# Optimization experiments

Hardware: AMD Instinct MI355X
Metric: run time of the kernel (lower is better)

## Reference

```python
import jax, jax.numpy as jnp
import numpy as np

LAYER_NUM = 2
NUM_CLS = 128
HIDDEN = 256
NUM_NODES = 1024


def setup_inputs() -> dict:
    key = jax.random.key(0)
    ks = jax.random.split(key, 12)
    s = 0.05
    return {
        "x": jax.random.normal(ks[0], (NUM_NODES, HIDDEN), jnp.float32),
        "knowledge": jax.random.uniform(ks[1], (NUM_CLS, NUM_CLS), jnp.float32) / NUM_CLS,
        "w3w": jax.random.normal(ks[2], (HIDDEN, 2 * HIDDEN), jnp.float32) * s,
        "b3w": jax.random.normal(ks[3], (HIDDEN,), jnp.float32) * s,
        "u3": jax.random.normal(ks[4], (HIDDEN, HIDDEN), jnp.float32) * s,
        "bu3": jax.random.normal(ks[5], (HIDDEN,), jnp.float32) * s,
        "w4w": jax.random.normal(ks[6], (HIDDEN, 2 * HIDDEN), jnp.float32) * s,
        "b4w": jax.random.normal(ks[7], (HIDDEN,), jnp.float32) * s,
        "w5w": jax.random.normal(ks[8], (HIDDEN, 2 * HIDDEN), jnp.float32) * s,
        "b5w": jax.random.normal(ks[9], (HIDDEN,), jnp.float32) * s,
        "u5": jax.random.normal(ks[10], (HIDDEN, HIDDEN), jnp.float32) * s,
        "bu5": jax.random.normal(ks[11], (HIDDEN,), jnp.float32) * s,
    }


def reference(x, knowledge, w3w, b3w, u3, bu3, w4w, b4w, w5w, b5w, u5, bu5):
    N, H = x.shape
    C = knowledge.shape[0]
    # hidden[n, c, :] = x[n, :]  (repeat per class)
    hidden = jnp.broadcast_to(x[:, None, :], (N, C, H))
    for _ in range(LAYER_NUM):
        hs = hidden.sum(0)                      # [C, H]
        diff = hs[None, :, :] - hidden          # [N, C, H]
        # knowledge.T @ diff_n  and  knowledge @ diff_n, vectorized over nodes
        left = jnp.einsum('kc,nkh->nch', knowledge, diff)
        right = jnp.einsum('ck,nkh->nch', knowledge, diff)
        av = jnp.concatenate([left, right], axis=-1).reshape(N * C, 2 * H)
        h = hidden.reshape(N * C, H)
        uh3 = h @ u3.T + bu3                    # shared: rv uses fc_eq3_u (source quirk)
        zv = jax.nn.sigmoid(av @ w3w.T + b3w + uh3)
        rv = jax.nn.sigmoid(av @ w4w.T + b4w + uh3)
        hv = jnp.tanh(av @ w5w.T + b5w + (rv * h) @ u5.T + bu5)
        h = (1.0 - zv) * h + zv * hv
        hidden = h.reshape(N, C, H)
    return hidden
```

## Files before the change

kernel.cpp:

```cpp
#include <hip/hip_runtime.h>
#include <cstdint>
#include <cstddef>


#define NODES 1024
#define NCLS  128
#define HID   256

using frag  = __attribute__((ext_vector_type(8))) short;
using frag4 = __attribute__((ext_vector_type(4))) short;
using f32x4 = __attribute__((ext_vector_type(4))) float;

__device__ __forceinline__ float bf2f(unsigned short h){
  unsigned int u = ((unsigned int)h) << 16;
  float f; __builtin_memcpy(&f, &u, 4); return f;
}
__device__ __forceinline__ unsigned short f2bf(float f){
  unsigned int u; __builtin_memcpy(&u, &f, 4);
  u = (u + 0x7fffu + ((u >> 16) & 1u)) >> 16;
  return (unsigned short)u;
}
__device__ __forceinline__ float sigm(float x){ return 1.0f/(1.0f + __expf(-x)); }
__device__ __forceinline__ float tanh_fast(float x){ return 1.0f - 2.0f/(__expf(2.0f*x) + 1.0f); }

#define GLOBAL_AS(p) ((const __attribute__((address_space(1))) void*)(p))
#define LDS_AS(p)    ((__attribute__((address_space(3))) void*)(p))

template<int OUT_BF16>
__global__ __launch_bounds__(256) void gemm_bf16(
    const unsigned short* __restrict__ A0, int ldA0, int K0,
    const unsigned short* __restrict__ A1, int ldA1,
    const unsigned short* __restrict__ BT, int ldB, long bStride,
    void* __restrict__ Cptr, int ldC,
    int Ntiles, int Ktot, unsigned int aMask, int Mtiles)
{
  __shared__ unsigned short As[4096];
  __shared__ unsigned short Bs[4096];
  const int t   = threadIdx.x;
  const int bid = blockIdx.x;
  const int xcd = bid & 7, slot = bid >> 3;
  const int mtPerX = (Mtiles >= 8) ? (Mtiles >> 3) : 1;
  const int mt = xcd * mtPerX + slot / Ntiles;
  const int nt = slot % Ntiles;
  const int lane = t & 63, w = t >> 6;
  const int wm = w >> 1, wn = w & 1;
  const int r = lane & 15, q = lane >> 4;
  const int m0 = mt * 128, n0 = nt * 128;
  const unsigned short* Bbase = BT + (size_t)mt * (size_t)bStride;

  f32x4 acc[4][4] = {};

  for (int kb = 0; kb < Ktot; kb += 32) {
#pragma unroll
    for (int i = 0; i < 2; ++i) {
      int u  = i * 256 + t;
      int mi = u >> 2;
      int kc = (u & 3) * 8;
      int k  = kb + kc;
      const unsigned short* ga;
      if (k < K0) ga = A0 + (size_t)((unsigned int)(m0 + mi) & aMask) * (size_t)ldA0 + k;
      else        ga = A1 + (size_t)(m0 + mi) * (size_t)ldA1 + (k - K0);
      __builtin_amdgcn_global_load_lds(GLOBAL_AS(ga), LDS_AS(&As[u * 8]), 16, 0, 0);
      const unsigned short* gb = Bbase + (size_t)(n0 + mi) * (size_t)ldB + k;
      __builtin_amdgcn_global_load_lds(GLOBAL_AS(gb), LDS_AS(&Bs[u * 8]), 16, 0, 0);
    }
    __syncthreads();

    frag af[4], bf_[4];
#pragma unroll
    for (int x = 0; x < 4; ++x) {
      af[x]  = *(const frag*)&As[(wm * 64 + x * 16 + r) * 32 + q * 8];
      bf_[x] = *(const frag*)&Bs[(wn * 64 + x * 16 + r) * 32 + q * 8];
    }
#pragma unroll
    for (int x = 0; x < 4; ++x)
#pragma unroll
      for (int y = 0; y < 4; ++y)
        acc[x][y] = __builtin_amdgcn_mfma_f32_16x16x32_bf16(af[x], bf_[y], acc[x][y], 0, 0, 0);
    __syncthreads();
  }

#pragma unroll
  for (int x = 0; x < 4; ++x) {
#pragma unroll
    for (int y = 0; y < 4; ++y) {
      int col = n0 + wn * 64 + y * 16 + r;
#pragma unroll
      for (int g = 0; g < 4; ++g) {
        long row = m0 + wm * 64 + x * 16 + q * 4 + g;
        if (OUT_BF16) ((unsigned short*)Cptr)[row * (long)ldC + col] = f2bf(acc[x][y][g]);
        else          ((float*)Cptr)[row * (long)ldC + col] = acc[x][y][g];
      }
    }
  }
}

__global__ __launch_bounds__(256, 4) void gemm_avh(
    const unsigned short* __restrict__ Ksrc, const unsigned short* __restrict__ H1T,
    unsigned short* __restrict__ AVH, int colOff)
{
  __shared__ unsigned short As[4096];
  __shared__ unsigned short Bs[4096];
  const int t   = threadIdx.x;
  const int bid = blockIdx.x;
  const int xcd = bid & 7, slot = bid >> 3;
  const int node = xcd * 128 + (slot >> 1);
  const int nt = slot & 1;
  const int lane = t & 63, w = t >> 6;
  const int wm = w >> 1, wn = w & 1;
  const int r = lane & 15, q = lane >> 4;
  const int n0 = nt * 128;
  const unsigned short* Bbase = H1T + (size_t)node * (HID * NCLS);

  f32x4 acc[4][4] = {};

  for (int kb = 0; kb < 128; kb += 32) {
#pragma unroll
    for (int i = 0; i < 2; ++i) {
      int u  = i * 256 + t;
      int mi = u >> 2;
      int kc = (u & 3) * 8;
      __builtin_amdgcn_global_load_lds(GLOBAL_AS(Ksrc + (size_t)mi * 128 + kb + kc),
                                       LDS_AS(&As[u * 8]), 16, 0, 0);
      __builtin_amdgcn_global_load_lds(GLOBAL_AS(Bbase + (size_t)(n0 + mi) * 128 + kb + kc),
                                       LDS_AS(&Bs[u * 8]), 16, 0, 0);
    }
    __syncthreads();

    frag af[4], bf_[4];
#pragma unroll
    for (int x = 0; x < 4; ++x) {
      af[x]  = *(const frag*)&As[(wm * 64 + x * 16 + r) * 32 + q * 8];
      bf_[x] = *(const frag*)&Bs[(wn * 64 + x * 16 + r) * 32 + q * 8];
    }
#pragma unroll
    for (int x = 0; x < 4; ++x)
#pragma unroll
      for (int y = 0; y < 4; ++y)
        acc[x][y] = __builtin_amdgcn_mfma_f32_16x16x32_bf16(af[x], bf_[y], acc[x][y], 0, 0, 0);
    __syncthreads();
  }

#pragma unroll
  for (int x = 0; x < 4; ++x) {
#pragma unroll
    for (int y = 0; y < 4; ++y) {
      int col = colOff + n0 + wn * 64 + y * 16 + r;
#pragma unroll
      for (int g = 0; g < 4; ++g) {
        long row = (long)node * 128 + wm * 64 + x * 16 + q * 4 + g;
        AVH[row * 512 + col] = f2bf(acc[x][y][g]);
      }
    }
  }
}

__global__ __launch_bounds__(256, 4) void gemm_pre(
    const unsigned short* __restrict__ AVH, const unsigned short* __restrict__ H1,
    const unsigned short* __restrict__ WB, unsigned short* __restrict__ PRE,
    int ctBase, int Ntiles, int Ktot)
{
  __shared__ unsigned short As[4096];
  __shared__ unsigned short Bs[4096];
  const int t   = threadIdx.x;
  const int bid = blockIdx.x;
  const int xcd = bid & 7, slot = bid >> 3;
  const int mt = xcd * 128 + slot / Ntiles;
  const int ct = ctBase + slot % Ntiles;
  const int lane = t & 63, w = t >> 6;
  const int wm = w >> 1, wn = w & 1;
  const int r = lane & 15, q = lane >> 4;
  const int m0 = mt * 128;
  const int mi = (2 * 256 + 0, t >> 2) ;
  (void)mi;

  f32x4 acc[4][4] = {};

  for (int kb = 0; kb < 512; kb += 32) {
#pragma unroll
    for (int i = 0; i < 2; ++i) {
      int u  = i * 256 + t;
      int m  = u >> 2;
      int kc = (u & 3) * 8;
      __builtin_amdgcn_global_load_lds(GLOBAL_AS(AVH + (size_t)(m0 + m) * 512 + kb + kc),
                                       LDS_AS(&As[u * 8]), 16, 0, 0);
      __builtin_amdgcn_global_load_lds(GLOBAL_AS(WB + (size_t)(ct * 128 + m) * 768 + kb + kc),
                                       LDS_AS(&Bs[u * 8]), 16, 0, 0);
    }
    __syncthreads();

    frag af[4], bf_[4];
#pragma unroll
    for (int x = 0; x < 4; ++x) {
      af[x]  = *(const frag*)&As[(wm * 64 + x * 16 + r) * 32 + q * 8];
      bf_[x] = *(const frag*)&Bs[(wn * 64 + x * 16 + r) * 32 + q * 8];
    }
#pragma unroll
    for (int x = 0; x < 4; ++x)
#pragma unroll
      for (int y = 0; y < 4; ++y)
        acc[x][y] = __builtin_amdgcn_mfma_f32_16x16x32_bf16(af[x], bf_[y], acc[x][y], 0, 0, 0);
    __syncthreads();
  }

  for (int kb = 512; kb < Ktot; kb += 32) {
#pragma unroll
    for (int i = 0; i < 2; ++i) {
      int u  = i * 256 + t;
      int m  = u >> 2;
      int kc = (u & 3) * 8;
      __builtin_amdgcn_global_load_lds(GLOBAL_AS(H1 + (size_t)(m0 + m) * 256 + (kb - 512) + kc),
                                       LDS_AS(&As[u * 8]), 16, 0, 0);
      __builtin_amdgcn_global_load_lds(GLOBAL_AS(WB + (size_t)(ct * 128 + m) * 768 + kb + kc),
                                       LDS_AS(&Bs[u * 8]), 16, 0, 0);
    }
    __syncthreads();

    frag af[4], bf_[4];
#pragma unroll
    for (int x = 0; x < 4; ++x) {
      af[x]  = *(const frag*)&As[(wm * 64 + x * 16 + r) * 32 + q * 8];
      bf_[x] = *(const frag*)&Bs[(wn * 64 + x * 16 + r) * 32 + q * 8];
    }
#pragma unroll
    for (int x = 0; x < 4; ++x)
#pragma unroll
      for (int y = 0; y < 4; ++y)
        acc[x][y] = __builtin_amdgcn_mfma_f32_16x16x32_bf16(af[x], bf_[y], acc[x][y], 0, 0, 0);
    __syncthreads();
  }

#pragma unroll
  for (int x = 0; x < 4; ++x) {
#pragma unroll
    for (int y = 0; y < 4; ++y) {
      int col = ct * 128 + wn * 64 + y * 16 + r;
#pragma unroll
      for (int g = 0; g < 4; ++g) {
        long row = m0 + wm * 64 + x * 16 + q * 4 + g;
        PRE[row * 768 + col] = f2bf(acc[x][y][g]);
      }
    }
  }
}

__global__ __launch_bounds__(256) void gemm_l1(
    const float* __restrict__ XW, const float* __restrict__ SW,
    const float* __restrict__ x,
    const float* __restrict__ b3, const float* __restrict__ b4,
    const float* __restrict__ b5, const float* __restrict__ bu3,
    const float* __restrict__ bu5,
    const float* __restrict__ colsum, const float* __restrict__ rowsum,
    const unsigned short* __restrict__ u5b,
    unsigned short* __restrict__ H1, unsigned short* __restrict__ H1T)
{
  __shared__ unsigned short As[4096], Bs[4096];
  __shared__ float tP1[256], tP2[256], tP3[256], tX[256];
  __shared__ float tZ1[256], tZ2[256], tZ3[256];
  __shared__ float tV1[256], tV2[256], tV3[256];
  __shared__ float tCS[128], tRS[128];

  const int t = threadIdx.x, bid = blockIdx.x;
  const int xcd = bid & 7, slot = bid >> 3;
  const int n  = xcd * 128 + (slot >> 1);
  const int nt = slot & 1;
  const int lane = t & 63, w = t >> 6, wm = w >> 1, wn = w & 1;
  const int r = lane & 15, q = lane >> 4;
  const int n0 = nt * 128;
  const float* xw = XW + (size_t)n * 1792;

  {
    int i = t;
    float xwi0 = xw[i], xwi1 = xw[256 + i], xwi2 = xw[512 + i], xwi3 = xw[768 + i];
    float xwi4 = xw[1024 + i], xwi5 = xw[1280 + i], xwu = xw[1536 + i];
    tP1[i] = SW[512 + i] - xwi2;
    tP2[i] = SW[768 + i] - xwi3;
    tP3[i] = xwu + b4[i] + bu3[i];
    tX[i]  = x[(size_t)n * HID + i];
    tZ1[i] = SW[i] - xwi0;
    tZ2[i] = SW[256 + i] - xwi1;
    tZ3[i] = xwu + b3[i] + bu3[i];
    tV1[i] = SW[1024 + i] - xwi4;
    tV2[i] = SW[1280 + i] - xwi5;
    tV3[i] = b5[i] + bu5[i];
    if (t < 128) { tCS[t] = colsum[t]; tRS[t] = rowsum[t]; }
  }
  __syncthreads();

  f32x4 acc[4][4] = {};

  for (int kb = 0; kb < 256; kb += 32) {
#pragma unroll
    for (int i = 0; i < 2; ++i) {
      int u  = i * 256 + t;
      int mi = u >> 2;
      int kc = (u & 3) * 8;
      int k  = kb + kc;
      __builtin_amdgcn_global_load_lds(GLOBAL_AS(u5b + (size_t)(n0 + mi) * 256 + k),
                                       LDS_AS(&Bs[u * 8]), 16, 0, 0);
      float cs = tCS[mi], rs = tRS[mi];
      frag a;
#pragma unroll
      for (int e = 0; e < 8; ++e) {
        int i2 = k + e;
        float pre = cs * tP1[i2] + rs * tP2[i2] + tP3[i2];
        a[e] = (short)f2bf(sigm(pre) * tX[i2]);
      }
      *(frag*)&As[u * 8] = a;
    }
    __syncthreads();

    frag af[4], bf_[4];
#pragma unroll
    for (int xx = 0; xx < 4; ++xx) {
      af[xx]  = *(const frag*)&As[(wm * 64 + xx * 16 + r) * 32 + q * 8];
      bf_[xx] = *(const frag*)&Bs[(wn * 64 + xx * 16 + r) * 32 + q * 8];
    }
#pragma unroll
    for (int xx = 0; xx < 4; ++xx)
#pragma unroll
      for (int y = 0; y < 4; ++y)
        acc[xx][y] = __builtin_amdgcn_mfma_f32_16x16x32_bf16(af[xx], bf_[y], acc[xx][y], 0, 0, 0);
    __syncthreads();
  }

#pragma unroll
  for (int xx = 0; xx < 4; ++xx) {
#pragma unroll
    for (int y = 0; y < 4; ++y) {
      int i = n0 + wn * 64 + y * 16 + r;
      frag4 pack;
#pragma unroll
      for (int g = 0; g < 4; ++g) {
        int c = wm * 64 + xx * 16 + q * 4 + g;
        float cs = tCS[c], rs = tRS[c];
        float z  = sigm(cs * tZ1[i] + rs * tZ2[i] + tZ3[i]);
        float p5 = cs * tV1[i] + rs * tV2[i] + tV3[i] + acc[xx][y][g];
        float h1 = (1.0f - z) * tX[i] + z * tanh_fast(p5);
        unsigned short hb = f2bf(h1);
        pack[g] = (short)hb;
        H1[(size_t)(n * 128 + c) * HID + i] = hb;
      }
      *(frag4*)(H1T + (size_t)n * (HID * NCLS) + (size_t)i * NCLS
                + (wm * 64 + xx * 16 + q * 4)) = pack;
    }
  }
}

__global__ __launch_bounds__(256) void gemm_l2(
    const unsigned short* __restrict__ PRE, const float* __restrict__ SG,
    const unsigned short* __restrict__ H1, const unsigned short* __restrict__ u5b,
    float* __restrict__ out)
{
  __shared__ unsigned short As[4096], Bs[4096];
  const int t = threadIdx.x, bid = blockIdx.x;
  const int xcd = bid & 7, slot = bid >> 3;
  const int mt = xcd * 128 + (slot >> 1);
  const int nt = slot & 1;
  const int lane = t & 63, w = t >> 6, wm = w >> 1, wn = w & 1;
  const int r = lane & 15, q = lane >> 4;
  const int m0 = mt * 128, n0 = nt * 128;

  f32x4 acc[4][4] = {};

  for (int kb = 0; kb < 256; kb += 32) {
#pragma unroll
    for (int i = 0; i < 2; ++i) {
      int u  = i * 256 + t;
      int mi = u >> 2;
      int kc = (u & 3) * 8;
      int k  = kb + kc;
      __builtin_amdgcn_global_load_lds(GLOBAL_AS(u5b + (size_t)(n0 + mi) * 256 + k),
                                       LDS_AS(&Bs[u * 8]), 16, 0, 0);
      long row = m0 + mi;
      frag p4 = *(const frag*)(PRE + row * 768 + 256 + k);
      frag h1 = *(const frag*)(H1 + row * 256 + k);
      const float* sg = SG + (size_t)mi * 768 + 256 + k;
      frag a;
#pragma unroll
      for (int e = 0; e < 8; ++e) {
        float rv = sigm(sg[e] + bf2f((unsigned short)p4[e]));
        a[e] = (short)f2bf(rv * bf2f((unsigned short)h1[e]));
      }
      *(frag*)&As[u * 8] = a;
    }
    __syncthreads();

    frag af[4], bf_[4];
#pragma unroll
    for (int xx = 0; xx < 4; ++xx) {
      af[xx]  = *(const frag*)&As[(wm * 64 + xx * 16 + r) * 32 + q * 8];
      bf_[xx] = *(const frag*)&Bs[(wn * 64 + xx * 16 + r) * 32 + q * 8];
    }
#pragma unroll
    for (int xx = 0; xx < 4; ++xx)
#pragma unroll
      for (int y = 0; y < 4; ++y)
        acc[xx][y] = __builtin_amdgcn_mfma_f32_16x16x32_bf16(af[xx], bf_[y], acc[xx][y], 0, 0, 0);
    __syncthreads();
  }

#pragma unroll
  for (int xx = 0; xx < 4; ++xx) {
#pragma unroll
    for (int y = 0; y < 4; ++y) {
      int i = n0 + wn * 64 + y * 16 + r;
#pragma unroll
      for (int g = 0; g < 4; ++g) {
        int c = wm * 64 + xx * 16 + q * 4 + g;
        long row = m0 + c;
        float z  = sigm(SG[(size_t)c * 768 + i] + bf2f(PRE[row * 768 + i]));
        float pv = SG[(size_t)c * 768 + 512 + i] + bf2f(PRE[row * 768 + 512 + i])
                 + acc[xx][y][g];
        float h  = bf2f(H1[row * 256 + i]);
        out[row * 256 + i] = (1.0f - z) * h + z * tanh_fast(pv);
      }
    }
  }
}

__global__ __launch_bounds__(256) void prep_cast(
    const float* __restrict__ x, const float* __restrict__ Kn,
    const float* __restrict__ w3, const float* __restrict__ u3,
    const float* __restrict__ w4, const float* __restrict__ w5,
    const float* __restrict__ u5,
    unsigned short* __restrict__ xb, unsigned short* __restrict__ WB,
    unsigned short* __restrict__ WB2, unsigned short* __restrict__ u5b,
    unsigned short* __restrict__ KbN, unsigned short* __restrict__ KTbN)
{
  int idx = blockIdx.x * 256 + threadIdx.x;
  if (idx < 262144) { xb[idx] = f2bf(x[idx]); return; }
  idx -= 262144;
  if (idx < 589824) {
    int col = idx / 768, j = idx % 768;
    int g = col >> 8, i = col & 255;
    float v;
    if (j < 512) { const float* wg = (g == 0) ? w3 : (g == 1) ? w4 : w5; v = wg[(size_t)i * 512 + j]; }
    else v = (g < 2) ? u3[(size_t)i * 256 + (j - 512)] : 0.0f;
    WB[(size_t)col * 768 + j] = f2bf(v);
    return;
  }
  idx -= 589824;
  if (idx < 458752) {
    int col = idx / 256, h = idx % 256;
    int b = col >> 8, i = col & 255;
    float v = (b < 6) ? ((b < 2 ? w3 : (b < 4 ? w4 : w5))[(size_t)i * 512 + (b & 1) * 256 + h])
                      : u3[(size_t)i * 256 + h];
    WB2[(size_t)col * 256 + h] = f2bf(v);
    return;
  }
  idx -= 458752;
  if (idx < 65536) { u5b[idx] = f2bf(u5[idx]); return; }
  idx -= 65536;
  if (idx < 16384) { int c = idx >> 7, k = idx & 127; KbN[idx]  = f2bf(-Kn[c * 128 + k]); return; }
  idx -= 16384;
  { int c = idx >> 7, k = idx & 127; KTbN[idx] = f2bf(-Kn[k * 128 + c]); }
}

__global__ __launch_bounds__(256) void prep_reduce(
    const float* __restrict__ x, const float* __restrict__ Kn,
    float* __restrict__ S, float* __restrict__ colsum, float* __restrict__ rowsum)
{
  int b = blockIdx.x, t = threadIdx.x;
  if (b < 8) {
    float s = 0.f;
    for (int n = 0; n < 128; ++n) s += x[(size_t)(b * 128 + n) * HID + t];
    atomicAdd(&S[t], s);
  } else if (b == 8) {
    if (t < NCLS) { float s = 0.f; for (int k = 0; k < NCLS; ++k) s += Kn[k * NCLS + t]; colsum[t] = s; }
  } else {
    if (t < NCLS) { float s = 0.f; for (int k = 0; k < NCLS; ++k) s += Kn[t * NCLS + k]; rowsum[t] = s; }
  }
}

__global__ __launch_bounds__(256) void prep_sw(
    const float* __restrict__ S, const float* __restrict__ w3,
    const float* __restrict__ w4, const float* __restrict__ w5, float* __restrict__ SW)
{
  int col = blockIdx.x * 256 + threadIdx.x;
  int b = col >> 8, i = col & 255;
  const float* w = (b < 2) ? w3 : (b < 4) ? w4 : w5;
  const float* row = w + (size_t)i * 512 + (b & 1) * 256;
  float s = 0.f;
  for (int h = 0; h < HID; ++h) s += S[h] * row[h];
  SW[col] = s;
}

__global__ __launch_bounds__(256) void reduce_hs(
    const unsigned short* __restrict__ H1, float* __restrict__ hs)
{
  int bid = blockIdx.x;
  int c = bid >> 5, nch = bid & 31;
  int i = threadIdx.x;
  const unsigned short* p = H1 + (size_t)nch * 32 * NCLS * HID + (size_t)c * HID + i;
  float s = 0.f;
  for (int n = 0; n < 32; ++n) s += bf2f(p[(size_t)n * NCLS * HID]);
  atomicAdd(&hs[c * HID + i], s);
}

__global__ __launch_bounds__(256) void p2a(
    const float* __restrict__ hs, const float* __restrict__ w3,
    const float* __restrict__ w4, const float* __restrict__ w5, float* __restrict__ hsW)
{
  __shared__ float hrow[HID];
  int k = blockIdx.x & 127, b = blockIdx.x >> 7;
  int t = threadIdx.x;
  hrow[t] = hs[k * HID + t];
  __syncthreads();
  const float* w = (b < 2) ? w3 : (b < 4) ? w4 : w5;
  const float* row = w + (size_t)t * 512 + (b & 1) * 256;
  float s = 0.f;
  for (int h = 0; h < HID; ++h) s += hrow[h] * row[h];
  hsW[(size_t)k * 1536 + b * 256 + t] = s;
}

__global__ __launch_bounds__(256) void p2b(
    const float* __restrict__ hsW, const float* __restrict__ Kn,
    const float* __restrict__ b3, const float* __restrict__ b4, const float* __restrict__ b5,
    const float* __restrict__ bu3, const float* __restrict__ bu5, float* __restrict__ SG)
{
  __shared__ float kc[NCLS], kr[NCLS];
  int c = blockIdx.x, t = threadIdx.x;
  if (t < NCLS) { kc[t] = Kn[t * NCLS + c]; kr[t] = Kn[c * NCLS + t]; }
  __syncthreads();
  for (int g = 0; g < 3; ++g) {
    int i = t;
    const float* L = hsW + (size_t)(2 * g) * 256 + i;
    const float* R = hsW + (size_t)(2 * g + 1) * 256 + i;
    float s = 0.f;
    for (int k = 0; k < NCLS; ++k) s += kc[k] * L[(size_t)k * 1536] + kr[k] * R[(size_t)k * 1536];
    const float* bg = (g == 0) ? b3 : (g == 1) ? b4 : b5;
    s += bg[i] + ((g < 2) ? bu3[i] : bu5[i]);
    SG[(size_t)c * 768 + g * 256 + i] = s;
  }
}

extern "C" void kernel_launch(void* const* d_in, const int* in_sizes, int n_in,
                              void* d_out, int out_size, void* d_ws, size_t ws_size,
                              hipStream_t stream) {
  (void)in_sizes; (void)n_in; (void)out_size; (void)ws_size;
  const float* x   = (const float*)d_in[0];
  const float* Kn  = (const float*)d_in[1];
  const float* w3  = (const float*)d_in[2];
  const float* b3  = (const float*)d_in[3];
  const float* u3  = (const float*)d_in[4];
  const float* bu3 = (const float*)d_in[5];
  const float* w4  = (const float*)d_in[6];
  const float* b4  = (const float*)d_in[7];
  const float* w5  = (const float*)d_in[8];
  const float* b5  = (const float*)d_in[9];
  const float* u5  = (const float*)d_in[10];
  const float* bu5 = (const float*)d_in[11];
  float* out = (float*)d_out;

  char* w = (char*)d_ws;
  unsigned short* AVH = (unsigned short*)(w);
  unsigned short* PRE = (unsigned short*)(w + 134217728);
  unsigned short* H1  = (unsigned short*)(w + 335544320);
  unsigned short* H1T = (unsigned short*)(w + 402653184);
  float*          XW  = (float*)(w + 469762048);
  char* misc = w + 477102080;
  float* S      = (float*)(misc);
  float* hs     = (float*)(misc + 1024);
  float* SW     = (float*)(misc + 132096);
  float* colsum = (float*)(misc + 138240);
  float* rowsum = (float*)(misc + 138752);
  float* hsW    = (float*)(misc + 139264);
  float* SG     = (float*)(misc + 925696);
  unsigned short* WB   = (unsigned short*)(misc + 1318912);
  unsigned short* WB2  = (unsigned short*)(misc + 2498560);
  unsigned short* u5b  = (unsigned short*)(misc + 3416064);
  unsigned short* KbN  = (unsigned short*)(misc + 3547136);
  unsigned short* KTbN = (unsigned short*)(misc + 3579904);
  unsigned short* xb   = (unsigned short*)(misc + 3612672);

  hipMemsetAsync(misc, 0, 132096, stream);

  prep_cast<<<5504, 256, 0, stream>>>(x, Kn, w3, u3, w4, w5, u5, xb, WB, WB2, u5b, KbN, KTbN);
  prep_reduce<<<10, 256, 0, stream>>>(x, Kn, S, colsum, rowsum);
  prep_sw<<<6, 256, 0, stream>>>(S, w3, w4, w5, SW);

  gemm_bf16<0><<<8 * 14, 256, 0, stream>>>(xb, 256, 256, xb, 256, WB2, 256, 0L,
                                           (void*)XW, 1792, 14, 256, 0xFFFFFFFFu, 8);
  gemm_l1<<<2048, 256, 0, stream>>>(XW, SW, x, b3, b4, b5, bu3, bu5,
                                    colsum, rowsum, u5b, H1, H1T);

  reduce_hs<<<4096, 256, 0, stream>>>(H1, hs);
  p2a<<<768, 256, 0, stream>>>(hs, w3, w4, w5, hsW);
  p2b<<<128, 256, 0, stream>>>(hsW, Kn, b3, b4, b5, bu3, bu5, SG);

  gemm_avh<<<2048, 256, 0, stream>>>(KTbN, H1T, AVH, 0);
  gemm_avh<<<2048, 256, 0, stream>>>(KbN, H1T, AVH, 256);

  gemm_pre<<<1024 * 4, 256, 0, stream>>>(AVH, H1, WB, PRE, 0, 4, 768);
  gemm_pre<<<1024 * 2, 256, 0, stream>>>(AVH, H1, WB, PRE, 4, 2, 512);

  gemm_l2<<<2048, 256, 0, stream>>>(PRE, SG, H1, u5b, out);
}
```

Baseline: 829.9 us.

## Fuse knowledge GEMMs into layer-1 epilogue, merge pre GEMM launches, swizzle LDS

The layer-1 kernel now keeps its output tile transposed in LDS and directly computes both knowledge-matrix products (K^T·h and K·h) into AVH. This removes the H1T global buffer and the two separate gemm_avh launches. The two gemm_pre launches are merged into one 6144-block launch that uses K=64 staging with XOR-swizzled LDS, and the other GEMM kernels gain XOR swizzles to reduce bank conflicts. In exchange, gemm_l1 needs more LDS, reads the knowledge fragments straight from global memory, and gemm_pre blocks now have uneven work per column tile.

```diff
diff --git a/kernel.cpp b/kernel.cpp
--- a/kernel.cpp
+++ b/kernel.cpp
@@ -95,139 +95,87 @@
   }
 }
 
-__global__ __launch_bounds__(256, 4) void gemm_avh(
-    const unsigned short* __restrict__ Ksrc, const unsigned short* __restrict__ H1T,
-    unsigned short* __restrict__ AVH, int colOff)
-{
-  __shared__ unsigned short As[4096];
-  __shared__ unsigned short Bs[4096];
+__global__ __launch_bounds__(256, 4) void gemm_pre(
+    const unsigned short* __restrict__ AVH, const unsigned short* __restrict__ H1,
+    const unsigned short* __restrict__ WB, unsigned short* __restrict__ PRE)
+{
+  __shared__ unsigned short As[8192];
+  __shared__ unsigned short Bs[8192];
   const int t   = threadIdx.x;
   const int bid = blockIdx.x;
   const int xcd = bid & 7, slot = bid >> 3;
-  const int node = xcd * 128 + (slot >> 1);
-  const int nt = slot & 1;
-  const int lane = t & 63, w = t >> 6;
-  const int wm = w >> 1, wn = w & 1;
-  const int r = lane & 15, q = lane >> 4;
-  const int n0 = nt * 128;
-  const unsigned short* Bbase = H1T + (size_t)node * (HID * NCLS);
-
-  f32x4 acc[4][4] = {};
-
-  for (int kb = 0; kb < 128; kb += 32) {
-#pragma unroll
-    for (int i = 0; i < 2; ++i) {
-      int u  = i * 256 + t;
-      int mi = u >> 2;
-      int kc = (u & 3) * 8;
-      __builtin_amdgcn_global_load_lds(GLOBAL_AS(Ksrc + (size_t)mi * 128 + kb + kc),
-                                       LDS_AS(&As[u * 8]), 16, 0, 0);
-      __builtin_amdgcn_global_load_lds(GLOBAL_AS(Bbase + (size_t)(n0 + mi) * 128 + kb + kc),
-                                       LDS_AS(&Bs[u * 8]), 16, 0, 0);
-    }
-    __syncthreads();
-
-    frag af[4], bf_[4];
-#pragma unroll
-    for (int x = 0; x < 4; ++x) {
-      af[x]  = *(const frag*)&As[(wm * 64 + x * 16 + r) * 32 + q * 8];
-      bf_[x] = *(const frag*)&Bs[(wn * 64 + x * 16 + r) * 32 + q * 8];
-    }
-#pragma unroll
-    for (int x = 0; x < 4; ++x)
-#pragma unroll
-      for (int y = 0; y < 4; ++y)
-        acc[x][y] = __builtin_amdgcn_mfma_f32_16x16x32_bf16(af[x], bf_[y], acc[x][y], 0, 0, 0);
-    __syncthreads();
-  }
-
-#pragma unroll
-  for (int x = 0; x < 4; ++x) {
-#pragma unroll
-    for (int y = 0; y < 4; ++y) {
-      int col = colOff + n0 + wn * 64 + y * 16 + r;
-#pragma unroll
-      for (int g = 0; g < 4; ++g) {
-        long row = (long)node * 128 + wm * 64 + x * 16 + q * 4 + g;
-        AVH[row * 512 + col] = f2bf(acc[x][y][g]);
-      }
-    }
-  }
-}
-
-__global__ __launch_bounds__(256, 4) void gemm_pre(
-    const unsigned short* __restrict__ AVH, const unsigned short* __restrict__ H1,
-    const unsigned short* __restrict__ WB, unsigned short* __restrict__ PRE,
-    int ctBase, int Ntiles, int Ktot)
-{
-  __shared__ unsigned short As[4096];
-  __shared__ unsigned short Bs[4096];
-  const int t   = threadIdx.x;
-  const int bid = blockIdx.x;
-  const int xcd = bid & 7, slot = bid >> 3;
-  const int mt = xcd * 128 + slot / Ntiles;
-  const int ct = ctBase + slot % Ntiles;
+  const int mt = xcd * 128 + slot / 6;
+  const int ct = slot % 6;
   const int lane = t & 63, w = t >> 6;
   const int wm = w >> 1, wn = w & 1;
   const int r = lane & 15, q = lane >> 4;
   const int m0 = mt * 128;
-  const int mi = (2 * 256 + 0, t >> 2) ;
-  (void)mi;
+  const unsigned short* Wrow = WB + (size_t)(ct * 128) * 768;
 
   f32x4 acc[4][4] = {};
 
-  for (int kb = 0; kb < 512; kb += 32) {
-#pragma unroll
-    for (int i = 0; i < 2; ++i) {
+  for (int kb = 0; kb < 512; kb += 64) {
+#pragma unroll
+    for (int i = 0; i < 4; ++i) {
       int u  = i * 256 + t;
-      int m  = u >> 2;
-      int kc = (u & 3) * 8;
-      __builtin_amdgcn_global_load_lds(GLOBAL_AS(AVH + (size_t)(m0 + m) * 512 + kb + kc),
+      int mi = u >> 3;
+      int gc = (u & 7) ^ (mi & 7);
+      __builtin_amdgcn_global_load_lds(GLOBAL_AS(AVH + (size_t)(m0 + mi) * 512 + kb + gc * 8),
                                        LDS_AS(&As[u * 8]), 16, 0, 0);
-      __builtin_amdgcn_global_load_lds(GLOBAL_AS(WB + (size_t)(ct * 128 + m) * 768 + kb + kc),
+      __builtin_amdgcn_global_load_lds(GLOBAL_AS(Wrow + (size_t)mi * 768 + kb + gc * 8),
                                        LDS_AS(&Bs[u * 8]), 16, 0, 0);
     }
     __syncthreads();
-
-    frag af[4], bf_[4];
-#pragma unroll
-    for (int x = 0; x < 4; ++x) {
-      af[x]  = *(const frag*)&As[(wm * 64 + x * 16 + r) * 32 + q * 8];
-      bf_[x] = *(const frag*)&Bs[(wn * 64 + x * 16 + r) * 32 + q * 8];
-    }
-#pragma unroll
-    for (int x = 0; x < 4; ++x)
-#pragma unroll
-      for (int y = 0; y < 4; ++y)
-        acc[x][y] = __builtin_amdgcn_mfma_f32_16x16x32_bf16(af[x], bf_[y], acc[x][y], 0, 0, 0);
-    __syncthreads();
-  }
-
-  for (int kb = 512; kb < Ktot; kb += 32) {
-#pragma unroll
-    for (int i = 0; i < 2; ++i) {
-      int u  = i * 256 + t;
-      int m  = u >> 2;
-      int kc = (u & 3) * 8;
-      __builtin_amdgcn_global_load_lds(GLOBAL_AS(H1 + (size_t)(m0 + m) * 256 + (kb - 512) + kc),
-                                       LDS_AS(&As[u * 8]), 16, 0, 0);
-      __builtin_amdgcn_global_load_lds(GLOBAL_AS(WB + (size_t)(ct * 128 + m) * 768 + kb + kc),
-                                       LDS_AS(&Bs[u * 8]), 16, 0, 0);
-    }
-    __syncthreads();
-
-    frag af[4], bf_[4];
-#pragma unroll
-    for (int x = 0; x < 4; ++x) {
-      af[x]  = *(const frag*)&As[(wm * 64 + x * 16 + r) * 32 + q * 8];
-      bf_[x] = *(const frag*)&Bs[(wn * 64 + x * 16 + r) * 32 + q * 8];
-    }
-#pragma unroll
-    for (int x = 0; x < 4; ++x)
-#pragma unroll
-      for (int y = 0; y < 4; ++y)
-        acc[x][y] = __builtin_amdgcn_mfma_f32_16x16x32_bf16(af[x], bf_[y], acc[x][y], 0, 0, 0);
-    __syncthreads();
+#pragma unroll
+    for (int kh = 0; kh < 2; ++kh) {
+      frag af[4], bf_[4];
+#pragma unroll
+      for (int x = 0; x < 4; ++x) {
+        int ra = wm * 64 + x * 16 + r;
+        int rb = wn * 64 + x * 16 + r;
+        af[x]  = *(const frag*)&As[ra * 64 + (((kh * 4 + q) ^ (ra & 7)) * 8)];
+        bf_[x] = *(const frag*)&Bs[rb * 64 + (((kh * 4 + q) ^ (rb & 7)) * 8)];
+      }
+#pragma unroll
+      for (int x = 0; x < 4; ++x)
+#pragma unroll
+        for (int y = 0; y < 4; ++y)
+          acc[x][y] = __builtin_amdgcn_mfma_f32_16x16x32_bf16(af[x], bf_[y], acc[x][y], 0, 0, 0);
+    }
+    __syncthreads();
+  }
+
+  if (ct < 4) {
+    for (int kb = 0; kb < 256; kb += 64) {
+#pragma unroll
+      for (int i = 0; i < 4; ++i) {
+        int u  = i * 256 + t;
+        int mi = u >> 3;
+        int gc = (u & 7) ^ (mi & 7);
+        __builtin_amdgcn_global_load_lds(GLOBAL_AS(H1 + (size_t)(m0 + mi) * 256 + kb + gc * 8),
+                                         LDS_AS(&As[u * 8]), 16, 0, 0);
+        __builtin_amdgcn_global_load_lds(GLOBAL_AS(Wrow + (size_t)mi * 768 + 512 + kb + gc * 8),
+                                         LDS_AS(&Bs[u * 8]), 16, 0, 0);
+      }
+      __syncthreads();
+#pragma unroll
+      for (int kh = 0; kh < 2; ++kh) {
+        frag af[4], bf_[4];
+#pragma unroll
+        for (int x = 0; x < 4; ++x) {
+          int ra = wm * 64 + x * 16 + r;
+          int rb = wn * 64 + x * 16 + r;
+          af[x]  = *(const frag*)&As[ra * 64 + (((kh * 4 + q) ^ (ra & 7)) * 8)];
+          bf_[x] = *(const frag*)&Bs[rb * 64 + (((kh * 4 + q) ^ (rb & 7)) * 8)];
+        }
+#pragma unroll
+        for (int x = 0; x < 4; ++x)
+#pragma unroll
+          for (int y = 0; y < 4; ++y)
+            acc[x][y] = __builtin_amdgcn_mfma_f32_16x16x32_bf16(af[x], bf_[y], acc[x][y], 0, 0, 0);
+      }
+      __syncthreads();
+    }
   }
 
 #pragma unroll
@@ -252,9 +200,13 @@
     const float* __restrict__ bu5,
     const float* __restrict__ colsum, const float* __restrict__ rowsum,
     const unsigned short* __restrict__ u5b,
-    unsigned short* __restrict__ H1, unsigned short* __restrict__ H1T)
-{
-  __shared__ unsigned short As[4096], Bs[4096];
+    const unsigned short* __restrict__ KTbN, const unsigned short* __restrict__ KbN,
+    unsigned short* __restrict__ H1, unsigned short* __restrict__ AVH)
+{
+  __shared__ unsigned short SM[17408];
+  unsigned short* As = SM;
+  unsigned short* Bs = SM + 4096;
+  unsigned short* L  = SM;
   __shared__ float tP1[256], tP2[256], tP3[256], tX[256];
   __shared__ float tZ1[256], tZ2[256], tZ3[256];
   __shared__ float tV1[256], tV2[256], tV3[256];
@@ -294,9 +246,11 @@
     for (int i = 0; i < 2; ++i) {
       int u  = i * 256 + t;
       int mi = u >> 2;
-      int kc = (u & 3) * 8;
+      int c  = u & 3;
+      int kc = c * 8;
       int k  = kb + kc;
-      __builtin_amdgcn_global_load_lds(GLOBAL_AS(u5b + (size_t)(n0 + mi) * 256 + k),
+      int gc = c ^ (mi & 3);
+      __builtin_amdgcn_global_load_lds(GLOBAL_AS(u5b + (size_t)(n0 + mi) * 256 + kb + gc * 8),
                                        LDS_AS(&Bs[u * 8]), 16, 0, 0);
       float cs = tCS[mi], rs = tRS[mi];
       frag a;
@@ -306,15 +260,17 @@
         float pre = cs * tP1[i2] + rs * tP2[i2] + tP3[i2];
         a[e] = (short)f2bf(sigm(pre) * tX[i2]);
       }
-      *(frag*)&As[u * 8] = a;
+      *(frag*)&As[mi * 32 + (c ^ (mi & 3)) * 8] = a;
     }
     __syncthreads();
 
     frag af[4], bf_[4];
 #pragma unroll
     for (int xx = 0; xx < 4; ++xx) {
-      af[xx]  = *(const frag*)&As[(wm * 64 + xx * 16 + r) * 32 + q * 8];
-      bf_[xx] = *(const frag*)&Bs[(wn * 64 + xx * 16 + r) * 32 + q * 8];
+      int ra = wm * 64 + xx * 16 + r;
+      int rb = wn * 64 + xx * 16 + r;
+      af[xx]  = *(const frag*)&As[ra * 32 + ((q ^ (ra & 3)) * 8)];
+      bf_[xx] = *(const frag*)&Bs[rb * 32 + ((q ^ (rb & 3)) * 8)];
     }
 #pragma unroll
     for (int xx = 0; xx < 4; ++xx)
@@ -328,7 +284,8 @@
   for (int xx = 0; xx < 4; ++xx) {
 #pragma unroll
     for (int y = 0; y < 4; ++y) {
-      int i = n0 + wn * 64 + y * 16 + r;
+      int j = wn * 64 + y * 16 + r;
+      int i = n0 + j;
       frag4 pack;
 #pragma unroll
       for (int g = 0; g < 4; ++g) {
@@ -341,9 +298,42 @@
         pack[g] = (short)hb;
         H1[(size_t)(n * 128 + c) * HID + i] = hb;
       }
-      *(frag4*)(H1T + (size_t)n * (HID * NCLS) + (size_t)i * NCLS
-                + (wm * 64 + xx * 16 + q * 4)) = pack;
-    }
+      *(frag4*)&L[j * 136 + (wm * 64 + xx * 16 + q * 4)] = pack;
+    }
+  }
+  __syncthreads();
+
+#pragma unroll
+  for (int s = 0; s < 2; ++s) {
+    const unsigned short* Ks = s ? KbN : KTbN;
+    f32x4 a2[4][4] = {};
+#pragma unroll
+    for (int kb = 0; kb < 4; ++kb) {
+      frag af[4], bf_[4];
+#pragma unroll
+      for (int xx = 0; xx < 4; ++xx) {
+        int cp = wm * 64 + xx * 16 + r;
+        af[xx] = *(const frag*)(Ks + (size_t)cp * 128 + kb * 32 + q * 8);
+        int j = wn * 64 + xx * 16 + r;
+        bf_[xx] = *(const frag*)&L[j * 136 + kb * 32 + q * 8];
+      }
+#pragma unroll
+      for (int xx = 0; xx < 4; ++xx)
+#pragma unroll
+        for (int y = 0; y < 4; ++y)
+          a2[xx][y] = __builtin_amdgcn_mfma_f32_16x16x32_bf16(af[xx], bf_[y], a2[xx][y], 0, 0, 0);
+    }
+#pragma unroll
+    for (int xx = 0; xx < 4; ++xx)
+#pragma unroll
+      for (int y = 0; y < 4; ++y) {
+        int col = s * 256 + n0 + wn * 64 + y * 16 + r;
+#pragma unroll
+        for (int g = 0; g < 4; ++g) {
+          int cp = wm * 64 + xx * 16 + q * 4 + g;
+          AVH[(size_t)(n * 128 + cp) * 512 + col] = f2bf(a2[xx][y][g]);
+        }
+      }
   }
 }
 
@@ -368,9 +358,10 @@
     for (int i = 0; i < 2; ++i) {
       int u  = i * 256 + t;
       int mi = u >> 2;
-      int kc = (u & 3) * 8;
-      int k  = kb + kc;
-      __builtin_amdgcn_global_load_lds(GLOBAL_AS(u5b + (size_t)(n0 + mi) * 256 + k),
+      int c  = u & 3;
+      int k  = kb + c * 8;
+      int gc = c ^ (mi & 3);
+      __builtin_amdgcn_global_load_lds(GLOBAL_AS(u5b + (size_t)(n0 + mi) * 256 + kb + gc * 8),
                                        LDS_AS(&Bs[u * 8]), 16, 0, 0);
       long row = m0 + mi;
       frag p4 = *(const frag*)(PRE + row * 768 + 256 + k);
@@ -382,15 +373,17 @@
         float rv = sigm(sg[e] + bf2f((unsigned short)p4[e]));
         a[e] = (short)f2bf(rv * bf2f((unsigned short)h1[e]));
       }
-      *(frag*)&As[u * 8] = a;
+      *(frag*)&As[mi * 32 + (c ^ (mi & 3)) * 8] = a;
     }
     __syncthreads();
 
     frag af[4], bf_[4];
 #pragma unroll
     for (int xx = 0; xx < 4; ++xx) {
-      af[xx]  = *(const frag*)&As[(wm * 64 + xx * 16 + r) * 32 + q * 8];
-      bf_[xx] = *(const frag*)&Bs[(wn * 64 + xx * 16 + r) * 32 + q * 8];
+      int ra = wm * 64 + xx * 16 + r;
+      int rb = wn * 64 + xx * 16 + r;
+      af[xx]  = *(const frag*)&As[ra * 32 + ((q ^ (ra & 3)) * 8)];
+      bf_[xx] = *(const frag*)&Bs[rb * 32 + ((q ^ (rb & 3)) * 8)];
     }
 #pragma unroll
     for (int xx = 0; xx < 4; ++xx)
@@ -557,9 +550,8 @@
   unsigned short* AVH = (unsigned short*)(w);
   unsigned short* PRE = (unsigned short*)(w + 134217728);
   unsigned short* H1  = (unsigned short*)(w + 335544320);
-  unsigned short* H1T = (unsigned short*)(w + 402653184);
-  float*          XW  = (float*)(w + 469762048);
-  char* misc = w + 477102080;
+  float*          XW  = (float*)(w + 402653184);
+  char* misc = w + 409993216;
   float* S      = (float*)(misc);
   float* hs     = (float*)(misc + 1024);
   float* SW     = (float*)(misc + 132096);
@@ -583,17 +575,13 @@
   gemm_bf16<0><<<8 * 14, 256, 0, stream>>>(xb, 256, 256, xb, 256, WB2, 256, 0L,
                                            (void*)XW, 1792, 14, 256, 0xFFFFFFFFu, 8);
   gemm_l1<<<2048, 256, 0, stream>>>(XW, SW, x, b3, b4, b5, bu3, bu5,
-                                    colsum, rowsum, u5b, H1, H1T);
+                                    colsum, rowsum, u5b, KTbN, KbN, H1, AVH);
 
   reduce_hs<<<4096, 256, 0, stream>>>(H1, hs);
   p2a<<<768, 256, 0, stream>>>(hs, w3, w4, w5, hsW);
   p2b<<<128, 256, 0, stream>>>(hsW, Kn, b3, b4, b5, bu3, bu5, SG);
 
-  gemm_avh<<<2048, 256, 0, stream>>>(KTbN, H1T, AVH, 0);
-  gemm_avh<<<2048, 256, 0, stream>>>(KbN, H1T, AVH, 256);
-
-  gemm_pre<<<1024 * 4, 256, 0, stream>>>(AVH, H1, WB, PRE, 0, 4, 768);
-  gemm_pre<<<1024 * 2, 256, 0, stream>>>(AVH, H1, WB, PRE, 4, 2, 512);
+  gemm_pre<<<6144, 256, 0, stream>>>(AVH, H1, WB, PRE);
 
   gemm_l2<<<2048, 256, 0, stream>>>(PRE, SG, H1, u5b, out);
 }
```

Result: faster. 776.5 us (-6.4%).
